# Kernel optimization log

Measured on AMD Instinct MI355X. Metric: run time of the kernel, lower is better.

The kernel has to match this reference:

```python
import jax, jax.numpy as jnp
import numpy as np

N = 10000   # nodes
E = 50000   # edges
G = 8       # graphs in batch
IN = 16     # input_dim
H = 64      # hidden_dim
EH = 32     # edge-network hidden
L = 3       # num ECC layers
BN_EPS = 1e-5


def _xavier(k, shape):
    fan_in, fan_out = shape[-2], shape[-1]
    s = jnp.sqrt(2.0 / (fan_in + fan_out)).astype(jnp.float32)
    return jax.random.normal(k, shape, jnp.float32) * s


def setup_inputs() -> dict:
    key = jax.random.key(0)
    ks = jax.random.split(key, 10)
    x = jax.random.normal(ks[0], (N, IN), jnp.float32)
    edge_index = jax.random.randint(ks[1], (2, E), 0, N, jnp.int32)
    batch = jnp.sort(jax.random.randint(ks[2], (N,), 0, G, jnp.int32))
    return {
        "x": x,
        "edge_index": edge_index,
        "batch": batch,
        "emb_w": _xavier(ks[3], (IN, H)),
        "emb_b": jnp.zeros((H,), jnp.float32),
        "e1_w": _xavier(ks[4], (L, 1, EH)),
        "e1_b": jnp.zeros((L, EH), jnp.float32),
        "e2_w": _xavier(ks[5], (L, EH, H * H)),
        "e2_b": jnp.zeros((L, H * H), jnp.float32),
        "self_w": _xavier(ks[6], (L, H, H)),
        "self_b": jnp.zeros((L, H), jnp.float32),
        "bn_g": jnp.ones((L, H), jnp.float32),
        "bn_b": jnp.zeros((L, H), jnp.float32),
        "cls_w": _xavier(ks[7], (2 * H, 1)),
        "cls_b": jnp.zeros((1,), jnp.float32),
    }


def reference(x, edge_index, batch, emb_w, emb_b, e1_w, e1_b, e2_w, e2_b,
              self_w, self_b, bn_g, bn_b, cls_w, cls_b):
    src, dst = edge_index[0], edge_index[1]
    # in-degree of targets for 'mean' aggregation (computed once; edge structure fixed)
    deg = jnp.clip(jax.ops.segment_sum(jnp.ones((E,), x.dtype), dst, num_segments=N), 1.0, None)

    h = x @ emb_w + emb_b  # [N, H] input embedding
    for l in range(L):
        # edge_attr: L2 distance between first 3 hidden channels of endpoints, [E,1]
        d = h[src, :3] - h[dst, :3]
        ea = jnp.sqrt(jnp.sum(d * d, axis=1, keepdims=True))
        # edge network -> per-edge dynamic weight matrix [E, H, H]
        hid = jax.nn.relu(ea @ e1_w[l] + e1_b[l])          # [E, EH]
        W = (hid @ e2_w[l] + e2_b[l]).reshape(E, H, H)
        # message: x_j (source features) times per-edge weight
        msg = jnp.einsum('ei,eio->eo', h[src], W)          # [E, H]
        agg = jax.ops.segment_sum(msg, dst, num_segments=N) / deg[:, None]
        h2 = agg + h @ self_w[l] + self_b[l]               # ECC output + self transform
        # BatchNorm1d (training-mode batch stats, biased variance), then ReLU
        mu = h2.mean(axis=0)
        var = h2.var(axis=0)
        h = jax.nn.relu(bn_g[l] * (h2 - mu) * jax.lax.rsqrt(var + BN_EPS) + bn_b[l])
        # dropout is a no-op in eval mode

    cnt = jnp.clip(jax.ops.segment_sum(jnp.ones((N,), h.dtype), batch, num_segments=G), 1.0, None)
    h_mean = jax.ops.segment_sum(h, batch, num_segments=G) / cnt[:, None]
    h_max = jax.ops.segment_max(h, batch, num_segments=G)
    h_pooled = jnp.concatenate([h_mean, h_max], axis=1)    # [G, 2H]
    return jax.nn.sigmoid(h_pooled @ cls_w + cls_b)        # [G, 1]
```

## Files before the change

### kernel.cpp

```cpp
#include <hip/hip_runtime.h>
#include <math.h>

#define N_NODES 10000
#define N_EDGES 50000
#define N_GRAPHS 8
#define IN_DIM  16
#define HID     64
#define EHID    32
#define NLAYER  3
#define NK      33
#define BN_EPS  1e-5f
#define POOL_BLOCKS 63
#define LAYER_BLOCKS 625

#define OFF_H0     0u
#define OFF_H2A    640000u
#define OFF_H2B    1280000u
#define OFF_ATAB   1920000u
#define OFF_CTAB   2325504u
#define OFF_S      2731008u
#define OFF_NB     2731136u
#define OFF_DEG    2731200u
#define OFF_ROWPTR 2741200u
#define OFF_CUR    2751248u
#define OFF_CSRC   2761248u
#define OFF_STATS  2811248u
#define OFF_GSUM   2811632u
#define OFF_GMAX   2812144u
#define OFF_GCNT   2812656u
#define OFF_CNTR   2812664u

__device__ __forceinline__ float rl(float v, int i) {
    return __int_as_float(__builtin_amdgcn_readlane(__float_as_int(v), i));
}

__device__ __forceinline__ void bn_coef(const float* __restrict__ sPrev,
                                        const float* __restrict__ gPrev,
                                        const float* __restrict__ bPrev,
                                        int c, float& sc, float& sf) {
    float mu  = sPrev[c] * (1.0f / N_NODES);
    float var = fmaf(-mu, mu, sPrev[64 + c] * (1.0f / N_NODES));
    float rstd = 1.0f / sqrtf(var + BN_EPS);
    sc = gPrev[c] * rstd;
    sf = fmaf(-sc, mu, bPrev[c]);
}

__global__ void k_prep(const float* __restrict__ e1w, const float* __restrict__ e1b,
                       float* __restrict__ s_arr, int* __restrict__ nb,
                       int* __restrict__ deg, int* __restrict__ cur,
                       float* __restrict__ stats,
                       float* __restrict__ gsum, float* __restrict__ gmax,
                       int* __restrict__ gcnt, int* __restrict__ counter) {
    int l = blockIdx.x;
    if (threadIdx.x == 0) {
        float t[EHID]; int c = 0;
        for (int j = 0; j < EHID; ++j) {
            float a = e1w[l * EHID + j], b = e1b[l * EHID + j];
            if ((a > 0.f && b < 0.f) || (a < 0.f && b > 0.f)) t[c++] = -b / a;
        }
        for (int i = 1; i < c; ++i) {
            float v = t[i]; int j = i - 1;
            while (j >= 0 && t[j] > v) { t[j + 1] = t[j]; --j; }
            t[j + 1] = v;
        }
        nb[l] = c;
        for (int i = 0; i < c; ++i) s_arr[l * NK + i] = t[i];
    }
    if (l == 0) {
        for (int i = threadIdx.x; i < N_NODES; i += 256) { deg[i] = 0; cur[i] = 0; }
    } else if (l == 1) {
        for (int i = threadIdx.x; i < N_GRAPHS * HID; i += 256) { gsum[i] = 0.f; gmax[i] = 0.f; }
        if (threadIdx.x < N_GRAPHS) gcnt[threadIdx.x] = 0;
        if (threadIdx.x == 0) *counter = 0;
    } else {
        for (int i = threadIdx.x; i < NLAYER * 128; i += 256) stats[i] = 0.f;
    }
}

__global__ void k_deg(const int* __restrict__ ei, int* __restrict__ deg) {
    int e = blockIdx.x * blockDim.x + threadIdx.x;
    if (e < N_EDGES) atomicAdd(&deg[ei[N_EDGES + e]], 1);
}

__global__ void k_scan(const int* __restrict__ deg, int* __restrict__ rowptr) {
    __shared__ int part[256];
    int t = threadIdx.x;
    int base = t * 40;
    int s = 0;
    for (int i = 0; i < 40; ++i) {
        int n = base + i;
        if (n < N_NODES) s += deg[n];
    }
    part[t] = s;
    __syncthreads();
    for (int off = 1; off < 256; off <<= 1) {
        int v = (t >= off) ? part[t - off] : 0;
        __syncthreads();
        part[t] += v;
        __syncthreads();
    }
    int run = (t == 0) ? 0 : part[t - 1];
    for (int i = 0; i < 40; ++i) {
        int n = base + i;
        if (n < N_NODES) { rowptr[n] = run; run += deg[n]; }
    }
    if (t == 255) rowptr[N_NODES] = part[255];
}

__global__ void k_fill(const int* __restrict__ ei, const int* __restrict__ rowptr,
                       int* __restrict__ cur, int* __restrict__ csrc) {
    int e = blockIdx.x * blockDim.x + threadIdx.x;
    if (e < N_EDGES) {
        int dst = ei[N_EDGES + e];
        int pos = rowptr[dst] + atomicAdd(&cur[dst], 1);
        csrc[pos] = ei[e];
    }
}

__global__ void k_s2(const float* __restrict__ e1w, const float* __restrict__ e1b,
                     const float* __restrict__ e2w, const float* __restrict__ e2b,
                     const float* __restrict__ s_arr, const int* __restrict__ nb,
                     float* __restrict__ Atab, float* __restrict__ Ctab) {
    int q = blockIdx.x, k = blockIdx.y, l = blockIdx.z;
    int nbl = nb[l];
    if (k > nbl) return;
    __shared__ float sma[EHID], smb[EHID];
    if (threadIdx.x < EHID) {
        float a = e1w[l * EHID + threadIdx.x], b = e1b[l * EHID + threadIdx.x];
        float lo = (k == 0) ? 0.f : s_arr[l * NK + k - 1];
        float hi = s_arr[l * NK + k];
        float p  = (k == nbl) ? (lo + 1.0f) : 0.5f * (lo + hi);
        float m  = (p * a + b > 0.f) ? 1.f : 0.f;
        sma[threadIdx.x] = m * a;
        smb[threadIdx.x] = m * b;
    }
    __syncthreads();
    int idx = q * 1024 + threadIdx.x * 4;
    const float4* w4base = (const float4*)(e2w);
    float4 accA = make_float4(0.f, 0.f, 0.f, 0.f);
    float4 accC = *(const float4*)(e2b + l * HID * HID + idx);
    #pragma unroll
    for (int j = 0; j < EHID; ++j) {
        float4 w = w4base[((l * EHID + j) * (HID * HID) + idx) >> 2];
        float ma = sma[j], mb = smb[j];
        accA.x = fmaf(ma, w.x, accA.x); accA.y = fmaf(ma, w.y, accA.y);
        accA.z = fmaf(ma, w.z, accA.z); accA.w = fmaf(ma, w.w, accA.w);
        accC.x = fmaf(mb, w.x, accC.x); accC.y = fmaf(mb, w.y, accC.y);
        accC.z = fmaf(mb, w.z, accC.z); accC.w = fmaf(mb, w.w, accC.w);
    }
    *(float4*)(Atab + (l * NK + k) * (HID * HID) + idx) = accA;
    *(float4*)(Ctab + (l * NK + k) * (HID * HID) + idx) = accC;
}

__global__ void k_embed(const float* __restrict__ x, const float* __restrict__ w,
                        const float* __restrict__ b, float* __restrict__ h0) {
    int idx = blockIdx.x * blockDim.x + threadIdx.x;
    int n = idx >> 6, o = idx & 63;
    const float* xr = x + n * IN_DIM;
    float acc = b[o];
    #pragma unroll
    for (int i = 0; i < IN_DIM; ++i) acc = fmaf(xr[i], w[i * HID + o], acc);
    h0[idx] = acc;
}

__global__ void __launch_bounds__(256, 2)
k_layer(const float* __restrict__ hb, int useBN,
        const float* __restrict__ sPrev, const float* __restrict__ gPrev,
        const float* __restrict__ bPrev,
        const int* __restrict__ rowptr, const int* __restrict__ csrc,
        const int* __restrict__ deg,
        const float* __restrict__ Atab, const float* __restrict__ Ctab,
        const float* __restrict__ s_arr, const int* __restrict__ nbp, int l,
        const float* __restrict__ sw_l, const float* __restrict__ sb_l,
        float* __restrict__ h2out, float* __restrict__ statsOut) {
    __shared__ float smW[3 * HID * HID];
    __shared__ float sRed[2][4][HID];
    int tid = threadIdx.x, wid = tid >> 6, lane = tid & 63;
    int nb = nbp[l];
    const float* A0 = Atab + l * NK * HID * HID;
    const float* C0 = Ctab + l * NK * HID * HID;
    {
        float4* s4 = (float4*)smW;
        const float4* w4 = (const float4*)sw_l;
        const float4* a4 = (const float4*)A0;
        const float4* c4 = (const float4*)C0;
        #pragma unroll
        for (int p = 0; p < 4; ++p) {
            int j = p * 256 + tid;
            s4[j] = w4[j];
            s4[1024 + j] = a4[j];
            s4[2048 + j] = c4[j];
        }
    }
    __syncthreads();
    float sc = 0.f, sf = 0.f;
    if (useBN) bn_coef(sPrev, gPrev, bPrev, lane, sc, sf);
    float sbv = sb_l[lane];
    float ls = 0.f, ls2 = 0.f;
    #pragma unroll
    for (int c = 0; c < 4; ++c) {
        int node = blockIdx.x * 16 + c * 4 + wid;
        int idx = node * HID + lane;
        float hv = hb[idx];
        if (useBN) hv = fmaxf(fmaf(sc, hv, sf), 0.f);
        int jb = rowptr[node], je = rowptr[node + 1];
        float p = 0.f, q = 0.f, aggv = 0.f;
        if (nb == 0) {
            for (int j = jb; j < je; ++j) {
                int src = csrc[j];
                float hs = hb[src * HID + lane];
                if (useBN) hs = fmaxf(fmaf(sc, hs, sf), 0.f);
                float diff = hs - hv;
                float d0 = rl(diff, 0), d1 = rl(diff, 1), d2 = rl(diff, 2);
                float ea = sqrtf(d0 * d0 + d1 * d1 + d2 * d2);
                p = fmaf(ea, hs, p);
                q += hs;
            }
        } else {
            for (int j = jb; j < je; ++j) {
                int src = csrc[j];
                float hs = hb[src * HID + lane];
                if (useBN) hs = fmaxf(fmaf(sc, hs, sf), 0.f);
                float diff = hs - hv;
                float d0 = rl(diff, 0), d1 = rl(diff, 1), d2 = rl(diff, 2);
                float ea = sqrtf(d0 * d0 + d1 * d1 + d2 * d2);
                int k = 0;
                for (int i = 0; i < nb; ++i) k += (ea > s_arr[l * NK + i]) ? 1 : 0;
                const float* A = Atab + (l * NK + k) * (HID * HID);
                const float* C = Ctab + (l * NK + k) * (HID * HID);
                float au = 0.f, cu = 0.f;
                for (int i = 0; i < HID; ++i) {
                    float hi = rl(hs, i);
                    au = fmaf(hi, A[i * HID + lane], au);
                    cu = fmaf(hi, C[i * HID + lane], cu);
                }
                aggv += fmaf(ea, au, cu);
            }
        }
        float acc = sbv, accA = 0.f;
        #pragma unroll
        for (int i = 0; i < HID; ++i) {
            float hi = rl(hv, i), pi = rl(p, i), qi = rl(q, i);
            acc  = fmaf(hi, smW[i * HID + lane], acc);
            accA = fmaf(pi, smW[HID * HID + i * HID + lane], accA);
            accA = fmaf(qi, smW[2 * HID * HID + i * HID + lane], accA);
        }
        if (nb != 0) accA = aggv;
        float invd = 1.0f / fmaxf((float)deg[node], 1.0f);
        float v = fmaf(accA, invd, acc);
        h2out[idx] = v;
        ls += v; ls2 = fmaf(v, v, ls2);
    }
    sRed[0][wid][lane] = ls;
    sRed[1][wid][lane] = ls2;
    __syncthreads();
    if (tid < HID) {
        float s  = sRed[0][0][tid] + sRed[0][1][tid] + sRed[0][2][tid] + sRed[0][3][tid];
        float s2 = sRed[1][0][tid] + sRed[1][1][tid] + sRed[1][2][tid] + sRed[1][3][tid];
        atomicAdd(&statsOut[tid], s);
        atomicAdd(&statsOut[64 + tid], s2);
    }
}

__global__ void k_bnpool(const float* __restrict__ h2cur, const float* __restrict__ s2,
                         const float* __restrict__ g2, const float* __restrict__ b2,
                         const int* __restrict__ batch,
                         float* __restrict__ gsum, float* __restrict__ gmax,
                         int* __restrict__ gcnt, int* __restrict__ counter,
                         const float* __restrict__ cw, const float* __restrict__ cb,
                         float* __restrict__ out) {
    int tid = threadIdx.x;
    int wid = (blockIdx.x * 256 + tid) >> 6, lane = tid & 63;
    float sc, sf; bn_coef(s2, g2, b2, lane, sc, sf);
    int n0 = wid * 40;
    int n1 = min(n0 + 40, N_NODES);
    float asum = 0.f, amax = 0.f;
    int cb2 = -1, run = 0;
    for (int n = n0; n < n1; ++n) {
        int b = batch[n];
        float v = fmaxf(fmaf(sc, h2cur[n * HID + lane], sf), 0.f);
        if (b != cb2) {
            if (cb2 >= 0) {
                atomicAdd(&gsum[cb2 * HID + lane], asum);
                atomicMax((int*)&gmax[cb2 * HID + lane], __float_as_int(amax));
                if (lane == 0) atomicAdd(&gcnt[cb2], run);
            }
            cb2 = b; asum = v; amax = v; run = 1;
        } else {
            asum += v; amax = fmaxf(amax, v); ++run;
        }
    }
    if (cb2 >= 0) {
        atomicAdd(&gsum[cb2 * HID + lane], asum);
        atomicMax((int*)&gmax[cb2 * HID + lane], __float_as_int(amax));
        if (lane == 0) atomicAdd(&gcnt[cb2], run);
    }
    __threadfence();
    __shared__ int lastFlag;
    if (tid == 0) {
        int old = __hip_atomic_fetch_add(counter, 1, __ATOMIC_ACQ_REL, __HIP_MEMORY_SCOPE_AGENT);
        lastFlag = (old == POOL_BLOCKS - 1);
    }
    __syncthreads();
    if (lastFlag && tid < N_GRAPHS) {
        int g = tid;
        float cnt = fmaxf((float)__hip_atomic_load(&gcnt[g], __ATOMIC_RELAXED, __HIP_MEMORY_SCOPE_AGENT), 1.f);
        float acc = cb[0];
        for (int o2 = 0; o2 < HID; ++o2) {
            float sv = __hip_atomic_load(&gsum[g * HID + o2], __ATOMIC_RELAXED, __HIP_MEMORY_SCOPE_AGENT);
            acc = fmaf(sv / cnt, cw[o2], acc);
        }
        for (int o2 = 0; o2 < HID; ++o2) {
            int iv = __hip_atomic_load((int*)&gmax[g * HID + o2], __ATOMIC_RELAXED, __HIP_MEMORY_SCOPE_AGENT);
            acc = fmaf(__int_as_float(iv), cw[HID + o2], acc);
        }
        out[g] = 1.0f / (1.0f + expf(-acc));
    }
}

extern "C" void kernel_launch(void* const* d_in, const int* in_sizes, int n_in,
                              void* d_out, int out_size, void* d_ws, size_t ws_size,
                              hipStream_t stream) {
    const float* x      = (const float*)d_in[0];
    const int*   ei     = (const int*)  d_in[1];
    const int*   batch  = (const int*)  d_in[2];
    const float* emb_w  = (const float*)d_in[3];
    const float* emb_b  = (const float*)d_in[4];
    const float* e1_w   = (const float*)d_in[5];
    const float* e1_b   = (const float*)d_in[6];
    const float* e2_w   = (const float*)d_in[7];
    const float* e2_b   = (const float*)d_in[8];
    const float* self_w = (const float*)d_in[9];
    const float* self_b = (const float*)d_in[10];
    const float* bn_g   = (const float*)d_in[11];
    const float* bn_b   = (const float*)d_in[12];
    const float* cls_w  = (const float*)d_in[13];
    const float* cls_b  = (const float*)d_in[14];
    float* out = (float*)d_out;

    float* wsf = (float*)d_ws;
    float* h0     = wsf + OFF_H0;
    float* h2a    = wsf + OFF_H2A;
    float* h2b    = wsf + OFF_H2B;
    float* Atab   = wsf + OFF_ATAB;
    float* Ctab   = wsf + OFF_CTAB;
    float* s_arr  = wsf + OFF_S;
    int*   nb     = (int*)(wsf + OFF_NB);
    int*   deg    = (int*)(wsf + OFF_DEG);
    int*   rowptr = (int*)(wsf + OFF_ROWPTR);
    int*   cur    = (int*)(wsf + OFF_CUR);
    int*   csrc   = (int*)(wsf + OFF_CSRC);
    float* stats  = wsf + OFF_STATS;
    float* gsum   = wsf + OFF_GSUM;
    float* gmax   = wsf + OFF_GMAX;
    int*   gcnt   = (int*)(wsf + OFF_GCNT);
    int*   cntr   = (int*)(wsf + OFF_CNTR);

    k_prep<<<NLAYER, 256, 0, stream>>>(e1_w, e1_b, s_arr, nb, deg, cur, stats, gsum, gmax, gcnt, cntr);
    k_deg<<<(N_EDGES + 255) / 256, 256, 0, stream>>>(ei, deg);
    k_scan<<<1, 256, 0, stream>>>(deg, rowptr);
    k_fill<<<(N_EDGES + 255) / 256, 256, 0, stream>>>(ei, rowptr, cur, csrc);
    k_s2<<<dim3(4, NK, NLAYER), 256, 0, stream>>>(e1_w, e1_b, e2_w, e2_b, s_arr, nb, Atab, Ctab);
    k_embed<<<(N_NODES * HID) / 256, 256, 0, stream>>>(x, emb_w, emb_b, h0);

    for (int l = 0; l < NLAYER; ++l) {
        const float* hb    = (l == 0) ? h0 : ((l == 1) ? h2a : h2b);
        float*       h2out = (l == 1) ? h2b : h2a;
        const float* sPrev = stats + (l - 1) * 128;
        const float* gPrev = bn_g + (l - 1) * HID;
        const float* bPrev = bn_b + (l - 1) * HID;
        int useBN = (l > 0);
        k_layer<<<LAYER_BLOCKS, 256, 0, stream>>>(hb, useBN, sPrev, gPrev, bPrev,
                                                  rowptr, csrc, deg,
                                                  Atab, Ctab, s_arr, nb, l,
                                                  self_w + l * HID * HID, self_b + l * HID,
                                                  h2out, stats + l * 128);
    }

    k_bnpool<<<POOL_BLOCKS, 256, 0, stream>>>(h2a, stats + 2 * 128, bn_g + 2 * HID, bn_b + 2 * HID,
                                              batch, gsum, gmax, gcnt, cntr, cls_w, cls_b, out);
}
```

Measured before the change: 182.0 us.

## Batch per-warp node transforms to reuse shared weights, unroll edge gathers

```diff
diff --git a/kernel.cpp b/kernel.cpp
--- a/kernel.cpp
+++ b/kernel.cpp
@@ -135,21 +135,21 @@
         smb[threadIdx.x] = m * b;
     }
     __syncthreads();
-    int idx = q * 1024 + threadIdx.x * 4;
+    int f4 = q * 64 + threadIdx.x;
     const float4* w4base = (const float4*)(e2w);
     float4 accA = make_float4(0.f, 0.f, 0.f, 0.f);
-    float4 accC = *(const float4*)(e2b + l * HID * HID + idx);
+    float4 accC = ((const float4*)(e2b + l * HID * HID))[f4];
     #pragma unroll
     for (int j = 0; j < EHID; ++j) {
-        float4 w = w4base[((l * EHID + j) * (HID * HID) + idx) >> 2];
+        float4 w = w4base[(l * EHID + j) * 1024 + f4];
         float ma = sma[j], mb = smb[j];
         accA.x = fmaf(ma, w.x, accA.x); accA.y = fmaf(ma, w.y, accA.y);
         accA.z = fmaf(ma, w.z, accA.z); accA.w = fmaf(ma, w.w, accA.w);
         accC.x = fmaf(mb, w.x, accC.x); accC.y = fmaf(mb, w.y, accC.y);
         accC.z = fmaf(mb, w.z, accC.z); accC.w = fmaf(mb, w.w, accC.w);
     }
-    *(float4*)(Atab + (l * NK + k) * (HID * HID) + idx) = accA;
-    *(float4*)(Ctab + (l * NK + k) * (HID * HID) + idx) = accC;
+    ((float4*)(Atab + (l * NK + k) * (HID * HID)))[f4] = accA;
+    ((float4*)(Ctab + (l * NK + k) * (HID * HID)))[f4] = accC;
 }
 
 __global__ void k_embed(const float* __restrict__ x, const float* __restrict__ w,
@@ -196,23 +196,43 @@
     float sc = 0.f, sf = 0.f;
     if (useBN) bn_coef(sPrev, gPrev, bPrev, lane, sc, sf);
     float sbv = sb_l[lane];
-    float ls = 0.f, ls2 = 0.f;
+    int nodeBase = blockIdx.x * 16 + wid * 4;
+
+    float hvv[4], pp[4], qq[4], aggE[4];
     #pragma unroll
     for (int c = 0; c < 4; ++c) {
-        int node = blockIdx.x * 16 + c * 4 + wid;
-        int idx = node * HID + lane;
-        float hv = hb[idx];
+        int node = nodeBase + c;
+        float hv = hb[node * HID + lane];
         if (useBN) hv = fmaxf(fmaf(sc, hv, sf), 0.f);
+        hvv[c] = hv;
+        float p = 0.f, q = 0.f, aggv = 0.f;
         int jb = rowptr[node], je = rowptr[node + 1];
-        float p = 0.f, q = 0.f, aggv = 0.f;
         if (nb == 0) {
-            for (int j = jb; j < je; ++j) {
-                int src = csrc[j];
-                float hs = hb[src * HID + lane];
+            int j = jb;
+            for (; j + 4 <= je; j += 4) {
+                int s0 = csrc[j], s1 = csrc[j + 1], s2 = csrc[j + 2], s3 = csrc[j + 3];
+                float h0 = hb[s0 * HID + lane];
+                float h1 = hb[s1 * HID + lane];
+                float h2 = hb[s2 * HID + lane];
+                float h3 = hb[s3 * HID + lane];
+                #pragma unroll
+                for (int u = 0; u < 4; ++u) {
+                    float hs = (u == 0) ? h0 : (u == 1) ? h1 : (u == 2) ? h2 : h3;
+                    if (useBN) hs = fmaxf(fmaf(sc, hs, sf), 0.f);
+                    float diff = hs - hv;
+                    float d0 = rl(diff, 0), d1 = rl(diff, 1), d2 = rl(diff, 2);
+                    float ea = sqrtf(fmaf(d0, d0, fmaf(d1, d1, d2 * d2)));
+                    p = fmaf(ea, hs, p);
+                    q += hs;
+                }
+            }
+            for (; j < je; ++j) {
+                int s = csrc[j];
+                float hs = hb[s * HID + lane];
                 if (useBN) hs = fmaxf(fmaf(sc, hs, sf), 0.f);
                 float diff = hs - hv;
                 float d0 = rl(diff, 0), d1 = rl(diff, 1), d2 = rl(diff, 2);
-                float ea = sqrtf(d0 * d0 + d1 * d1 + d2 * d2);
+                float ea = sqrtf(fmaf(d0, d0, fmaf(d1, d1, d2 * d2)));
                 p = fmaf(ea, hs, p);
                 q += hs;
             }
@@ -223,7 +243,7 @@
                 if (useBN) hs = fmaxf(fmaf(sc, hs, sf), 0.f);
                 float diff = hs - hv;
                 float d0 = rl(diff, 0), d1 = rl(diff, 1), d2 = rl(diff, 2);
-                float ea = sqrtf(d0 * d0 + d1 * d1 + d2 * d2);
+                float ea = sqrtf(fmaf(d0, d0, fmaf(d1, d1, d2 * d2)));
                 int k = 0;
                 for (int i = 0; i < nb; ++i) k += (ea > s_arr[l * NK + i]) ? 1 : 0;
                 const float* A = Atab + (l * NK + k) * (HID * HID);
@@ -237,18 +257,32 @@
                 aggv += fmaf(ea, au, cu);
             }
         }
-        float acc = sbv, accA = 0.f;
+        pp[c] = p; qq[c] = q; aggE[c] = aggv;
+    }
+
+    float acc[4], agg[4];
+    #pragma unroll
+    for (int c = 0; c < 4; ++c) { acc[c] = sbv; agg[c] = 0.f; }
+    #pragma unroll
+    for (int i = 0; i < HID; ++i) {
+        float ws = smW[i * HID + lane];
+        float wa = smW[HID * HID + i * HID + lane];
+        float wc = smW[2 * HID * HID + i * HID + lane];
         #pragma unroll
-        for (int i = 0; i < HID; ++i) {
-            float hi = rl(hv, i), pi = rl(p, i), qi = rl(q, i);
-            acc  = fmaf(hi, smW[i * HID + lane], acc);
-            accA = fmaf(pi, smW[HID * HID + i * HID + lane], accA);
-            accA = fmaf(qi, smW[2 * HID * HID + i * HID + lane], accA);
-        }
-        if (nb != 0) accA = aggv;
+        for (int c = 0; c < 4; ++c) {
+            acc[c] = fmaf(rl(hvv[c], i), ws, acc[c]);
+            agg[c] = fmaf(rl(pp[c], i), wa, agg[c]);
+            agg[c] = fmaf(rl(qq[c], i), wc, agg[c]);
+        }
+    }
+
+    float ls = 0.f, ls2 = 0.f;
+    #pragma unroll
+    for (int c = 0; c < 4; ++c) {
+        int node = nodeBase + c;
         float invd = 1.0f / fmaxf((float)deg[node], 1.0f);
-        float v = fmaf(accA, invd, acc);
-        h2out[idx] = v;
+        float v = fmaf(agg[c] + aggE[c], invd, acc[c]);
+        h2out[node * HID + lane] = v;
         ls += v; ls2 = fmaf(v, v, ls2);
     }
     sRed[0][wid][lane] = ls;
@@ -360,7 +394,7 @@
     k_deg<<<(N_EDGES + 255) / 256, 256, 0, stream>>>(ei, deg);
     k_scan<<<1, 256, 0, stream>>>(deg, rowptr);
     k_fill<<<(N_EDGES + 255) / 256, 256, 0, stream>>>(ei, rowptr, cur, csrc);
-    k_s2<<<dim3(4, NK, NLAYER), 256, 0, stream>>>(e1_w, e1_b, e2_w, e2_b, s_arr, nb, Atab, Ctab);
+    k_s2<<<dim3(16, NK, NLAYER), 64, 0, stream>>>(e1_w, e1_b, e2_w, e2_b, s_arr, nb, Atab, Ctab);
     k_embed<<<(N_NODES * HID) / 256, 256, 0, stream>>>(x, emb_w, emb_b, h0);
 
     for (int l = 0; l < NLAYER; ++l) {
```

Result: faster. 173.4 us (-4.8%).
